# Kernel tuning notes

Measured on AMD Instinct MI355X. Metric: run time of the kernel, lower is better.

Reference implementation:

```python
import jax, jax.numpy as jnp
import numpy as np

B, S, D, N, L, V = 2, 512, 1024, 4096, 4, 32000
EPS = 1e-5

def ternarize(w):
    # BitNet b1.58-style: scale = mean |w|, quantize to {-1,0,1}, rescale.
    s = jnp.mean(jnp.abs(w)) + 1e-8
    return s * jnp.round(jnp.clip(w / s, -1.0, 1.0))

def tern_ste(w):
    # straight-through estimator (faithful to ternary training)
    return w + jax.lax.stop_gradient(ternarize(w) - w)

def layer_norm(x, g, b):
    mu = jnp.mean(x, axis=-1, keepdims=True)
    var = jnp.var(x, axis=-1, keepdims=True)
    return (x - mu) * jax.lax.rsqrt(var + EPS) * g + b

def setup_inputs() -> dict:
    key = jax.random.key(0)
    ks = jax.random.split(key, 20)
    sc = lambda d: 1.0 / np.sqrt(d)
    inp = {
        'input_ids': jax.random.randint(ks[0], (B, S), 0, V, dtype=jnp.int32),
        'emb':       jax.random.normal(ks[1], (V, D), jnp.float32) * 0.02,
        'pos_emb':   jax.random.normal(ks[2], (S, D), jnp.float32) * 0.02,
        'gru_wih':   jax.random.normal(ks[3], (3 * D, D), jnp.float32) * sc(D),
        'gru_whh':   jax.random.normal(ks[4], (3 * D, D), jnp.float32) * sc(D),
        'gru_bih':   jnp.zeros((3 * D,), jnp.float32),
        'gru_bhh':   jnp.zeros((3 * D,), jnp.float32),
        'syn_w':     jax.random.normal(ks[5], (L, N, D), jnp.float32) * sc(D),
        'syn_b':     jnp.zeros((L, N), jnp.float32),
        'out_w':     jax.random.normal(ks[6], (L, D, N), jnp.float32) * sc(N),
        'out_b':     jnp.zeros((L, D), jnp.float32),
        'ln_g':      jnp.ones((L, D), jnp.float32),
        'ln_b':      jnp.zeros((L, D), jnp.float32),
        'on_g':      jnp.ones((D,), jnp.float32),
        'on_b':      jnp.zeros((D,), jnp.float32),
        'head_w':    jax.random.normal(ks[7], (V, D), jnp.float32) * sc(D),
        'head_b':    jnp.zeros((V,), jnp.float32),
    }
    return inp

def gru(x, wih, whh, bih, bhh):
    # x: [B,S,D] -> [B,S,D], torch nn.GRU semantics, h0 = 0
    # Precompute input projections for all timesteps: [B,S,3D]
    gi_all = jnp.einsum('bsd,ed->bse', x, wih) + bih
    def step(h, gi):
        gh = h @ whh.T + bhh
        ir, iz, inn = jnp.split(gi, 3, axis=-1)
        hr, hz, hn = jnp.split(gh, 3, axis=-1)
        r = jax.nn.sigmoid(ir + hr)
        z = jax.nn.sigmoid(iz + hz)
        n = jnp.tanh(inn + r * hn)
        h_new = (1.0 - z) * n + z * h
        return h_new, h_new
    h0 = jnp.zeros((x.shape[0], whh.shape[1]), x.dtype)
    _, hs = jax.lax.scan(step, h0, jnp.swapaxes(gi_all, 0, 1))
    return jnp.swapaxes(hs, 0, 1)

def reference(input_ids, emb, pos_emb, gru_wih, gru_whh, gru_bih, gru_bhh,
              syn_w, syn_b, out_w, out_b, ln_g, ln_b, on_g, on_b,
              head_w, head_b):
    # Ternary embedding lookup
    x = tern_ste(emb)[input_ids]                       # [B,S,D]
    x = x + pos_emb[None, :x.shape[1], :]
    x = gru(x, gru_wih, gru_whh, gru_bih, gru_bhh)
    for l in range(L):
        residual = x
        hidden = jax.nn.relu(jnp.einsum('bsd,nd->bsn', x, tern_ste(syn_w[l])) + syn_b[l])
        out = jnp.einsum('bsn,dn->bsd', hidden, tern_ste(out_w[l])) + out_b[l]
        x = layer_norm(residual + out, ln_g[l], ln_b[l])
    x = layer_norm(x, on_g, on_b)
    logits = jnp.einsum('bsd,vd->bsv', x, tern_ste(head_w)) + head_b  # [B,S,V]
    return logits
```

## Files before the change

### kernel.cpp

```cpp
#include <hip/hip_runtime.h>
#include <hip/hip_bf16.h>
#include <cstdint>
#include <cstddef>

#define Dm 1024
#define Sm 512
#define Bm 2
#define Nm 4096
#define Lm 4
#define Vm 32000

typedef __attribute__((ext_vector_type(8))) short short8;
typedef __attribute__((ext_vector_type(4))) float floatx4;

__device__ __forceinline__ unsigned short f2b(float f){
  union { float f; unsigned u; } v; v.f = f;
  unsigned r = (v.u + 0x7fffu + ((v.u >> 16) & 1u)) >> 16;
  return (unsigned short)r;
}

__device__ __forceinline__ float tern_thresh(double s64){
  float T = (float)(s64 * 0.5);
  if ((double)T > s64 * 0.5) T = __uint_as_float(__float_as_uint(T) - 1u);
  return T;
}

struct AbsumArgs { const float* src[10]; long n4[10]; };

__global__ __launch_bounds__(256) void absum_all_kernel(
    AbsumArgs a, double* __restrict__ parts)
{
  int slot = blockIdx.y;
  const float* x = a.src[slot];
  long n4 = a.n4[slot];
  long i = (long)blockIdx.x * blockDim.x + threadIdx.x;
  long stride = (long)gridDim.x * blockDim.x;
  double s = 0.0;
  for (; i < n4; i += stride){
    float4 v = ((const float4*)x)[i];
    s += (double)fabsf(v.x) + (double)fabsf(v.y)
       + (double)fabsf(v.z) + (double)fabsf(v.w);
  }
  #pragma unroll
  for (int off = 32; off; off >>= 1) s += __shfl_down(s, off, 64);
  __shared__ double wsum[4];
  int lane = threadIdx.x & 63, wv = threadIdx.x >> 6;
  if (lane == 0) wsum[wv] = s;
  __syncthreads();
  if (threadIdx.x == 0)
    parts[(size_t)slot * 512 + blockIdx.x] = wsum[0]+wsum[1]+wsum[2]+wsum[3];
}

__global__ __launch_bounds__(256) void absum_final_kernel(
    const double* __restrict__ part, double* __restrict__ scales)
{
  const double* p = part + (size_t)blockIdx.x * 512;
  int tid = threadIdx.x;
  double s = p[tid] + p[tid + 256];
  #pragma unroll
  for (int off = 32; off; off >>= 1) s += __shfl_down(s, off, 64);
  __shared__ double wsum[4];
  int lane = tid & 63, wv = tid >> 6;
  if (lane == 0) wsum[wv] = s;
  __syncthreads();
  if (tid == 0) scales[blockIdx.x] = wsum[0]+wsum[1]+wsum[2]+wsum[3];
}

struct PackArgs {
  const float* src[10]; unsigned short* dst[10];
  long n4[10]; int sidx[10]; double cnt[10];
};

__global__ __launch_bounds__(256) void pack_all_kernel(
    PackArgs a, const double* __restrict__ scales)
{
  int slot = blockIdx.y;
  const float* src = a.src[slot];
  unsigned short* dst = a.dst[slot];
  long n4 = a.n4[slot];
  bool tern = (a.sidx[slot] >= 0);
  float T = 0.f;
  if (tern){
    double s64 = scales[a.sidx[slot]] / a.cnt[slot] + 1e-8;
    T = tern_thresh(s64);
  }
  long i = (long)blockIdx.x * blockDim.x + threadIdx.x;
  long stride = (long)gridDim.x * blockDim.x;
  for (; i < n4; i += stride){
    float4 v = ((const float4*)src)[i];
    ushort4 u;
    if (tern){
      u.x = (v.x > T) ? 0x3F80 : ((v.x < -T) ? 0xBF80 : 0);
      u.y = (v.y > T) ? 0x3F80 : ((v.y < -T) ? 0xBF80 : 0);
      u.z = (v.z > T) ? 0x3F80 : ((v.z < -T) ? 0xBF80 : 0);
      u.w = (v.w > T) ? 0x3F80 : ((v.w < -T) ? 0xBF80 : 0);
    } else {
      u.x = f2b(v.x); u.y = f2b(v.y); u.z = f2b(v.z); u.w = f2b(v.w);
    }
    ((ushort4*)dst)[i] = u;
  }
}

__global__ __launch_bounds__(256) void embed_kernel(
    const int* __restrict__ ids, const float* __restrict__ emb,
    const float* __restrict__ pos, const double* __restrict__ ssum,
    unsigned short* __restrict__ xb)
{
  int row = blockIdx.x;
  int sp  = row & (Sm - 1);
  int id  = ids[row];
  double s64 = ssum[0] / ((double)Vm * (double)Dm) + 1e-8;
  float s = (float)s64;
  float T = tern_thresh(s64);
  int d = threadIdx.x * 4;
  float4 wv = *(const float4*)(emb + (size_t)id * Dm + d);
  float4 pv = *(const float4*)(pos + (size_t)sp * Dm + d);
  float q0 = (wv.x > T) ? 1.f : ((wv.x < -T) ? -1.f : 0.f);
  float q1 = (wv.y > T) ? 1.f : ((wv.y < -T) ? -1.f : 0.f);
  float q2 = (wv.z > T) ? 1.f : ((wv.z < -T) ? -1.f : 0.f);
  float q3 = (wv.w > T) ? 1.f : ((wv.w < -T) ? -1.f : 0.f);
  float y0 = s * q0 + pv.x;
  float y1 = s * q1 + pv.y;
  float y2 = s * q2 + pv.z;
  float y3 = s * q3 + pv.w;
  ushort4 u = make_ushort4(f2b(y0), f2b(y1), f2b(y2), f2b(y3));
  *(ushort4*)(xb + (size_t)row * Dm + d) = u;
}

template<int WM>
__global__ __launch_bounds__(256) void gemm_t(
    const unsigned short* __restrict__ A, const void* __restrict__ Wp,
    const float* __restrict__ bias, const double* __restrict__ ssum, double cnt,
    int relu, float* __restrict__ outf, unsigned short* __restrict__ outb,
    int M, int N, int K)
{
  __shared__ unsigned short As[128][40];
  __shared__ unsigned short Bs[128][40];
  int tid = threadIdx.x;
  int wave = tid >> 6, lane = tid & 63;
  int wm = wave >> 1, wn = wave & 1;
  int bm = blockIdx.y, bn = blockIdx.x;

  float s = 1.f, T = 0.f;
  if (ssum){
    double s64 = ssum[0] / cnt + 1e-8;
    s = (float)s64;
    T = tern_thresh(s64);
  }

  int arow = tid >> 1, achunk = tid & 1;
  const unsigned short* Ag = A + (size_t)(bm * 128 + arow) * K + achunk * 16;
  const float* Wg32 = (const float*)Wp + (size_t)(bn * 128 + arow) * K + achunk * 16;
  const unsigned short* Wg16 = (const unsigned short*)Wp + (size_t)(bn * 128 + arow) * K + achunk * 16;

  floatx4 acc[4][4];
  #pragma unroll
  for (int i = 0; i < 4; i++)
    #pragma unroll
    for (int j = 0; j < 4; j++)
      acc[i][j] = (floatx4){0.f, 0.f, 0.f, 0.f};

  for (int k0 = 0; k0 < K; k0 += 32){
    __syncthreads();
    uint4 a0 = *(const uint4*)(Ag + k0);
    uint4 a1 = *(const uint4*)(Ag + k0 + 8);
    *(uint4*)&As[arow][achunk * 16]     = a0;
    *(uint4*)&As[arow][achunk * 16 + 8] = a1;
    if (WM == 2){
      uint4 b0 = *(const uint4*)(Wg16 + k0);
      uint4 b1 = *(const uint4*)(Wg16 + k0 + 8);
      *(uint4*)&Bs[arow][achunk * 16]     = b0;
      *(uint4*)&Bs[arow][achunk * 16 + 8] = b1;
    } else {
      unsigned short tmp[16];
      #pragma unroll
      for (int q = 0; q < 4; q++){
        float4 wv = *(const float4*)(Wg32 + k0 + q * 4);
        if (WM == 1){
          tmp[q*4+0] = (wv.x > T) ? 0x3F80 : ((wv.x < -T) ? 0xBF80 : 0);
          tmp[q*4+1] = (wv.y > T) ? 0x3F80 : ((wv.y < -T) ? 0xBF80 : 0);
          tmp[q*4+2] = (wv.z > T) ? 0x3F80 : ((wv.z < -T) ? 0xBF80 : 0);
          tmp[q*4+3] = (wv.w > T) ? 0x3F80 : ((wv.w < -T) ? 0xBF80 : 0);
        } else {
          tmp[q*4+0] = f2b(wv.x); tmp[q*4+1] = f2b(wv.y);
          tmp[q*4+2] = f2b(wv.z); tmp[q*4+3] = f2b(wv.w);
        }
      }
      *(uint4*)&Bs[arow][achunk * 16]     = *(uint4*)&tmp[0];
      *(uint4*)&Bs[arow][achunk * 16 + 8] = *(uint4*)&tmp[8];
    }
    __syncthreads();

    int kq = lane >> 4, mr = lane & 15;
    short8 af[4], bf[4];
    #pragma unroll
    for (int i = 0; i < 4; i++) af[i] = *(const short8*)&As[wm*64 + i*16 + mr][kq*8];
    #pragma unroll
    for (int j = 0; j < 4; j++) bf[j] = *(const short8*)&Bs[wn*64 + j*16 + mr][kq*8];
    #pragma unroll
    for (int i = 0; i < 4; i++)
      #pragma unroll
      for (int j = 0; j < 4; j++)
        acc[i][j] = __builtin_amdgcn_mfma_f32_16x16x32_bf16(af[i], bf[j], acc[i][j], 0, 0, 0);
  }

  int cr = lane >> 4, cc = lane & 15;
  #pragma unroll
  for (int j = 0; j < 4; j++){
    int col = bn * 128 + wn * 64 + j * 16 + cc;
    float bv = bias ? bias[col] : 0.f;
    #pragma unroll
    for (int i = 0; i < 4; i++){
      #pragma unroll
      for (int r = 0; r < 4; r++){
        int row = bm * 128 + wm * 64 + i * 16 + cr * 4 + r;
        float v = acc[i][j][r] * s + bv;
        if (relu) v = fmaxf(v, 0.f);
        size_t idx = (size_t)row * N + col;
        if (outf) outf[idx] = v;
        if (outb) outb[idx] = f2b(v);
      }
    }
  }
}

template<int WM>
__global__ __launch_bounds__(256) void gemm_ks_t(
    const unsigned short* __restrict__ A, const void* __restrict__ Wp,
    const float* __restrict__ bias, const double* __restrict__ ssum, double cnt,
    float* __restrict__ p0, float* __restrict__ pext,
    int M, int N, int K, int Klen)
{
  __shared__ unsigned short As[128][40];
  __shared__ unsigned short Bs[128][40];
  int tid = threadIdx.x;
  int wave = tid >> 6, lane = tid & 63;
  int wm = wave >> 1, wn = wave & 1;
  int bm = blockIdx.y, bn = blockIdx.x, z = blockIdx.z;

  float s = 1.f, T = 0.f;
  if (ssum){
    double s64 = ssum[0] / cnt + 1e-8;
    s = (float)s64;
    T = tern_thresh(s64);
  }

  int arow = tid >> 1, achunk = tid & 1;
  int kbase = z * Klen;
  const unsigned short* Ag = A + (size_t)(bm * 128 + arow) * K + kbase + achunk * 16;
  const float* Wg32 = (const float*)Wp + (size_t)(bn * 128 + arow) * K + kbase + achunk * 16;
  const unsigned short* Wg16 = (const unsigned short*)Wp + (size_t)(bn * 128 + arow) * K + kbase + achunk * 16;

  floatx4 acc[4][4];
  #pragma unroll
  for (int i = 0; i < 4; i++)
    #pragma unroll
    for (int j = 0; j < 4; j++)
      acc[i][j] = (floatx4){0.f, 0.f, 0.f, 0.f};

  for (int k0 = 0; k0 < Klen; k0 += 32){
    __syncthreads();
    uint4 a0 = *(const uint4*)(Ag + k0);
    uint4 a1 = *(const uint4*)(Ag + k0 + 8);
    *(uint4*)&As[arow][achunk * 16]     = a0;
    *(uint4*)&As[arow][achunk * 16 + 8] = a1;
    if (WM == 2){
      uint4 b0 = *(const uint4*)(Wg16 + k0);
      uint4 b1 = *(const uint4*)(Wg16 + k0 + 8);
      *(uint4*)&Bs[arow][achunk * 16]     = b0;
      *(uint4*)&Bs[arow][achunk * 16 + 8] = b1;
    } else {
      unsigned short tmp[16];
      #pragma unroll
      for (int q = 0; q < 4; q++){
        float4 wv = *(const float4*)(Wg32 + k0 + q * 4);
        tmp[q*4+0] = (wv.x > T) ? 0x3F80 : ((wv.x < -T) ? 0xBF80 : 0);
        tmp[q*4+1] = (wv.y > T) ? 0x3F80 : ((wv.y < -T) ? 0xBF80 : 0);
        tmp[q*4+2] = (wv.z > T) ? 0x3F80 : ((wv.z < -T) ? 0xBF80 : 0);
        tmp[q*4+3] = (wv.w > T) ? 0x3F80 : ((wv.w < -T) ? 0xBF80 : 0);
      }
      *(uint4*)&Bs[arow][achunk * 16]     = *(uint4*)&tmp[0];
      *(uint4*)&Bs[arow][achunk * 16 + 8] = *(uint4*)&tmp[8];
    }
    __syncthreads();

    int kq = lane >> 4, mr = lane & 15;
    short8 af[4], bf[4];
    #pragma unroll
    for (int i = 0; i < 4; i++) af[i] = *(const short8*)&As[wm*64 + i*16 + mr][kq*8];
    #pragma unroll
    for (int j = 0; j < 4; j++) bf[j] = *(const short8*)&Bs[wn*64 + j*16 + mr][kq*8];
    #pragma unroll
    for (int i = 0; i < 4; i++)
      #pragma unroll
      for (int j = 0; j < 4; j++)
        acc[i][j] = __builtin_amdgcn_mfma_f32_16x16x32_bf16(af[i], bf[j], acc[i][j], 0, 0, 0);
  }

  float* outp = (z == 0) ? p0 : pext + (size_t)(z - 1) * M * N;
  int cr = lane >> 4, cc = lane & 15;
  #pragma unroll
  for (int j = 0; j < 4; j++){
    int col = bn * 128 + wn * 64 + j * 16 + cc;
    float bv = (z == 0 && bias) ? bias[col] : 0.f;
    #pragma unroll
    for (int i = 0; i < 4; i++){
      #pragma unroll
      for (int r = 0; r < 4; r++){
        int row = bm * 128 + wm * 64 + i * 16 + cr * 4 + r;
        outp[(size_t)row * N + col] = acc[i][j][r] * s + bv;
      }
    }
  }
}

template<int WM>
__global__ __launch_bounds__(512) void gemm256_t(
    const unsigned short* __restrict__ A, const void* __restrict__ Wp,
    const float* __restrict__ bias, const double* __restrict__ ssum, double cnt,
    int relu, float* __restrict__ outf, unsigned short* __restrict__ outb,
    int M, int N, int K)
{
  __shared__ unsigned short As[256][40];
  __shared__ unsigned short Bs[128][40];
  int tid = threadIdx.x;
  int wave = tid >> 6, lane = tid & 63;
  int wm = wave >> 1, wn = wave & 1;
  int bm = blockIdx.y, bn = blockIdx.x;

  float s = 1.f, T = 0.f;
  if (ssum){
    double s64 = ssum[0] / cnt + 1e-8;
    s = (float)s64;
    T = tern_thresh(s64);
  }

  int arow = tid >> 1, achunk = tid & 1;
  int wrow = tid >> 2, wchunk = tid & 3;
  const unsigned short* Ag = A + (size_t)(bm * 256 + arow) * K + achunk * 16;
  const float* Wg32 = (const float*)Wp + (size_t)(bn * 128 + wrow) * K + wchunk * 8;
  const unsigned short* Wg16 = (const unsigned short*)Wp + (size_t)(bn * 128 + wrow) * K + wchunk * 8;

  floatx4 acc[4][4];
  #pragma unroll
  for (int i = 0; i < 4; i++)
    #pragma unroll
    for (int j = 0; j < 4; j++)
      acc[i][j] = (floatx4){0.f, 0.f, 0.f, 0.f};

  for (int k0 = 0; k0 < K; k0 += 32){
    __syncthreads();
    uint4 a0 = *(const uint4*)(Ag + k0);
    uint4 a1 = *(const uint4*)(Ag + k0 + 8);
    *(uint4*)&As[arow][achunk * 16]     = a0;
    *(uint4*)&As[arow][achunk * 16 + 8] = a1;
    if (WM == 2){
      uint4 b0 = *(const uint4*)(Wg16 + k0);
      *(uint4*)&Bs[wrow][wchunk * 8] = b0;
    } else {
      unsigned short tmp[8];
      float4 w0 = *(const float4*)(Wg32 + k0);
      float4 w1 = *(const float4*)(Wg32 + k0 + 4);
      if (WM == 1){
        tmp[0] = (w0.x > T) ? 0x3F80 : ((w0.x < -T) ? 0xBF80 : 0);
        tmp[1] = (w0.y > T) ? 0x3F80 : ((w0.y < -T) ? 0xBF80 : 0);
        tmp[2] = (w0.z > T) ? 0x3F80 : ((w0.z < -T) ? 0xBF80 : 0);
        tmp[3] = (w0.w > T) ? 0x3F80 : ((w0.w < -T) ? 0xBF80 : 0);
        tmp[4] = (w1.x > T) ? 0x3F80 : ((w1.x < -T) ? 0xBF80 : 0);
        tmp[5] = (w1.y > T) ? 0x3F80 : ((w1.y < -T) ? 0xBF80 : 0);
        tmp[6] = (w1.z > T) ? 0x3F80 : ((w1.z < -T) ? 0xBF80 : 0);
        tmp[7] = (w1.w > T) ? 0x3F80 : ((w1.w < -T) ? 0xBF80 : 0);
      } else {
        tmp[0] = f2b(w0.x); tmp[1] = f2b(w0.y); tmp[2] = f2b(w0.z); tmp[3] = f2b(w0.w);
        tmp[4] = f2b(w1.x); tmp[5] = f2b(w1.y); tmp[6] = f2b(w1.z); tmp[7] = f2b(w1.w);
      }
      *(uint2*)&Bs[wrow][wchunk * 8]     = *(uint2*)&tmp[0];
      *(uint2*)&Bs[wrow][wchunk * 8 + 4] = *(uint2*)&tmp[4];
    }
    __syncthreads();

    int kq = lane >> 4, mr = lane & 15;
    short8 af[4], bf[4];
    #pragma unroll
    for (int i = 0; i < 4; i++) af[i] = *(const short8*)&As[wm*64 + i*16 + mr][kq*8];
    #pragma unroll
    for (int j = 0; j < 4; j++) bf[j] = *(const short8*)&Bs[wn*64 + j*16 + mr][kq*8];
    #pragma unroll
    for (int i = 0; i < 4; i++)
      #pragma unroll
      for (int j = 0; j < 4; j++)
        acc[i][j] = __builtin_amdgcn_mfma_f32_16x16x32_bf16(af[i], bf[j], acc[i][j], 0, 0, 0);
  }

  int cr = lane >> 4, cc = lane & 15;
  #pragma unroll
  for (int j = 0; j < 4; j++){
    int col = bn * 128 + wn * 64 + j * 16 + cc;
    float bv = bias ? bias[col] : 0.f;
    #pragma unroll
    for (int i = 0; i < 4; i++){
      #pragma unroll
      for (int r = 0; r < 4; r++){
        int row = bm * 256 + wm * 64 + i * 16 + cr * 4 + r;
        float v = acc[i][j][r] * s + bv;
        if (relu) v = fmaxf(v, 0.f);
        size_t idx = (size_t)row * N + col;
        if (outf) outf[idx] = v;
        if (outb) outb[idx] = f2b(v);
      }
    }
  }
}

__global__ __launch_bounds__(512) void gru_kernel(
    const float* __restrict__ gi, const float* __restrict__ whh, const float* __restrict__ bhh,
    unsigned long long* __restrict__ hbuf,
    float* __restrict__ hs, unsigned short* __restrict__ hsb)
{
  __shared__ __align__(16) float lds_h[2][Dm];
  __shared__ float lds_gh[24];
  int w = blockIdx.x, tid = threadIdx.x;
  int bb = w & 1, slice = w >> 1;
  int d0 = slice * 8;
  int o = tid >> 4, c = tid & 15;
  bool active = (o < 24);
  int g = o >> 3, dl = o & 7;
  int wrow = g * Dm + d0 + dl;
  float4 wr0 = {0,0,0,0}, wr1 = wr0, wr2 = wr0, wr3 = wr0,
         wr4 = wr0, wr5 = wr0, wr6 = wr0, wr7 = wr0,
         wr8 = wr0, wr9 = wr0, wr10 = wr0, wr11 = wr0,
         wr12 = wr0, wr13 = wr0, wr14 = wr0, wr15 = wr0;
  if (active){
    const float* wsrc = whh + (size_t)wrow * Dm + c * 4;
    wr0  = *(const float4*)(wsrc +  0*64);  wr1  = *(const float4*)(wsrc +  1*64);
    wr2  = *(const float4*)(wsrc +  2*64);  wr3  = *(const float4*)(wsrc +  3*64);
    wr4  = *(const float4*)(wsrc +  4*64);  wr5  = *(const float4*)(wsrc +  5*64);
    wr6  = *(const float4*)(wsrc +  6*64);  wr7  = *(const float4*)(wsrc +  7*64);
    wr8  = *(const float4*)(wsrc +  8*64);  wr9  = *(const float4*)(wsrc +  9*64);
    wr10 = *(const float4*)(wsrc + 10*64);  wr11 = *(const float4*)(wsrc + 11*64);
    wr12 = *(const float4*)(wsrc + 12*64);  wr13 = *(const float4*)(wsrc + 13*64);
    wr14 = *(const float4*)(wsrc + 14*64);  wr15 = *(const float4*)(wsrc + 15*64);
  }
  float bhval = (active && c == 0) ? bhh[wrow] : 0.f;

  int gidx = tid * 2;
  bool self = ((tid >> 2) == slice);
  int dd = tid;
  int dth = d0 + (tid & 7);
  float pir = 0.f, piz = 0.f, pin = 0.f;
  if (tid < 8){
    const float* girow = gi + (size_t)bb * Sm * (3 * Dm);
    pir = girow[dth]; piz = girow[Dm + dth]; pin = girow[2*Dm + dth];
  }

  for (int t = 0; t < Sm; t++){
    float* lh = lds_h[t & 1];
    if (!self || t == 0){
      const unsigned long long* hsrc = hbuf + (size_t)(t & 1) * 2048 + bb * 1024 + gidx;
      unsigned long long e0, e1;
      int spins = 0;
      for (;;){
        e0 = __hip_atomic_load(hsrc + 0, __ATOMIC_RELAXED, __HIP_MEMORY_SCOPE_AGENT);
        e1 = __hip_atomic_load(hsrc + 1, __ATOMIC_RELAXED, __HIP_MEMORY_SCOPE_AGENT);
        if (((unsigned)(e0 >> 32) == (unsigned)t) &&
            ((unsigned)(e1 >> 32) == (unsigned)t)) break;
        __builtin_amdgcn_s_sleep(2);
        if (++spins > (1 << 16)) break;
      }
      lh[gidx + 0] = __uint_as_float((unsigned)e0);
      lh[gidx + 1] = __uint_as_float((unsigned)e1);
    }
    __syncthreads();
    float acc = 0.f;
    if (active){
      const float* hb = lh + c * 4;
      float4 hv;
      #define GDOT(J, W) hv = *(const float4*)(hb + (J)*64); \
          acc += W.x*hv.x + W.y*hv.y + W.z*hv.z + W.w*hv.w;
      GDOT(0,wr0)  GDOT(1,wr1)  GDOT(2,wr2)  GDOT(3,wr3)
      GDOT(4,wr4)  GDOT(5,wr5)  GDOT(6,wr6)  GDOT(7,wr7)
      GDOT(8,wr8)  GDOT(9,wr9)  GDOT(10,wr10) GDOT(11,wr11)
      GDOT(12,wr12) GDOT(13,wr13) GDOT(14,wr14) GDOT(15,wr15)
      #undef GDOT
    }
    #pragma unroll
    for (int off = 8; off; off >>= 1) acc += __shfl_xor(acc, off, 16);
    if (active && c == 0) lds_gh[o] = acc + bhval;
    __syncthreads();
    if (tid < 8){
      float gr = lds_gh[dd];
      float gz = lds_gh[8 + dd];
      float gn = lds_gh[16 + dd];
      float hv = lh[dth];
      float rr = 1.f / (1.f + expf(-(pir + gr)));
      float zz = 1.f / (1.f + expf(-(piz + gz)));
      float nn = tanhf(pin + rr * gn);
      float hnew = (1.f - zz) * nn + zz * hv;
      unsigned long long pack =
          ((unsigned long long)(unsigned)(t + 1) << 32) | (unsigned long long)__float_as_uint(hnew);
      __hip_atomic_store(hbuf + (size_t)((t + 1) & 1) * 2048 + bb * 1024 + dth, pack,
                         __ATOMIC_RELAXED, __HIP_MEMORY_SCOPE_AGENT);
      lds_h[(t + 1) & 1][dth] = hnew;
      if (t + 1 < Sm){
        const float* girow = gi + ((size_t)bb * Sm + (t+1)) * (3 * Dm);
        pir = girow[dth]; piz = girow[Dm + dth]; pin = girow[2*Dm + dth];
      }
      size_t oi = ((size_t)bb * Sm + t) * Dm + dth;
      hs[oi]  = hnew;
      hsb[oi] = f2b(hnew);
    }
  }
}

__global__ __launch_bounds__(256) void ln_kernel(
    float* __restrict__ resid, const float* __restrict__ p0,
    const float* __restrict__ pext,
    const float* __restrict__ g, const float* __restrict__ b,
    float* __restrict__ outf, unsigned short* __restrict__ outb)
{
  int row = blockIdx.x;
  int d = threadIdx.x * 4;
  size_t base = (size_t)row * Dm + d;
  float4 v = *(float4*)(resid + base);
  if (p0){
    float4 a = *(const float4*)(p0 + base);
    v.x += a.x; v.y += a.y; v.z += a.z; v.w += a.w;
  }
  if (pext){
    const size_t stride = (size_t)1024 * Dm;
    #pragma unroll
    for (int e = 0; e < 3; e++){
      float4 a = *(const float4*)(pext + e * stride + base);
      v.x += a.x; v.y += a.y; v.z += a.z; v.w += a.w;
    }
  }
  float sum = v.x + v.y + v.z + v.w;
  float sq  = v.x*v.x + v.y*v.y + v.z*v.z + v.w*v.w;
  #pragma unroll
  for (int off = 32; off; off >>= 1){
    sum += __shfl_down(sum, off, 64);
    sq  += __shfl_down(sq,  off, 64);
  }
  __shared__ float red[4][2];
  __shared__ float bc[2];
  int lane = threadIdx.x & 63, wv = threadIdx.x >> 6;
  if (lane == 0){ red[wv][0] = sum; red[wv][1] = sq; }
  __syncthreads();
  if (threadIdx.x == 0){
    float st = red[0][0] + red[1][0] + red[2][0] + red[3][0];
    float qt = red[0][1] + red[1][1] + red[2][1] + red[3][1];
    float mu = st * (1.f / Dm);
    float var = qt * (1.f / Dm) - mu * mu;
    bc[0] = mu; bc[1] = rsqrtf(var + 1e-5f);
  }
  __syncthreads();
  float mu = bc[0], rs = bc[1];
  float4 gv = *(const float4*)(g + d);
  float4 bv = *(const float4*)(b + d);
  float4 y;
  y.x = (v.x - mu) * rs * gv.x + bv.x;
  y.y = (v.y - mu) * rs * gv.y + bv.y;
  y.z = (v.z - mu) * rs * gv.z + bv.z;
  y.w = (v.w - mu) * rs * gv.w + bv.w;
  if (outf) *(float4*)(outf + base) = y;
  if (outb){
    ushort4 u = make_ushort4(f2b(y.x), f2b(y.y), f2b(y.z), f2b(y.w));
    *(ushort4*)(outb + base) = u;
  }
}

extern "C" void kernel_launch(void* const* d_in, const int* in_sizes, int n_in,
                              void* d_out, int out_size, void* d_ws, size_t ws_size,
                              hipStream_t stream)
{
  const int*   ids    = (const int*)  d_in[0];
  const float* emb    = (const float*)d_in[1];
  const float* pos    = (const float*)d_in[2];
  const float* wih    = (const float*)d_in[3];
  const float* whh    = (const float*)d_in[4];
  const float* bih    = (const float*)d_in[5];
  const float* bhh    = (const float*)d_in[6];
  const float* syn_w  = (const float*)d_in[7];
  const float* syn_b  = (const float*)d_in[8];
  const float* out_w  = (const float*)d_in[9];
  const float* out_b  = (const float*)d_in[10];
  const float* ln_g   = (const float*)d_in[11];
  const float* ln_b   = (const float*)d_in[12];
  const float* on_g   = (const float*)d_in[13];
  const float* on_b   = (const float*)d_in[14];
  const float* head_w = (const float*)d_in[15];
  const float* head_b = (const float*)d_in[16];
  float* logits = (float*)d_out;

  char* ws = (char*)d_ws;
  double*             scales = (double*)ws;
  unsigned long long* hbuf   = (unsigned long long*)(ws + 4096);
  double*             parts  = (double*)(ws + 36864);
  unsigned short*     xb     = (unsigned short*)(ws + 131072);
  float*              hs     = (float*)(ws + ((size_t)4  << 20));
  unsigned short*     hidden = (unsigned short*)(ws + ((size_t)12 << 20));
  float*              outbuf = (float*)(ws + ((size_t)20 << 20));
  float*              gi     = (float*)(ws + ((size_t)24 << 20));
  unsigned short*     wih_b  = (unsigned short*)(ws + ((size_t)36 << 20));
  unsigned short*     syn_bk = (unsigned short*)(ws + ((size_t)42 << 20));
  unsigned short*     out_bk = (unsigned short*)(ws + ((size_t)74 << 20));
  unsigned short*     head_bk= (unsigned short*)(ws + ((size_t)106 << 20));
  const size_t NEED = ((size_t)106 << 20) + (size_t)Vm * Dm * 2;
  const bool packed = (ws_size >= NEED);

  hipMemsetAsync(d_ws, 0, 36864, stream);

  const double cnt_nd = (double)Nm * (double)Dm;
  const double cnt_vd = (double)Vm * (double)Dm;

  {
    AbsumArgs aa;
    aa.src[0] = emb;    aa.n4[0] = (long)Vm * Dm / 4;
    for (int l = 0; l < Lm; l++){
      aa.src[1 + l] = syn_w + (size_t)l * Nm * Dm; aa.n4[1 + l] = (long)Nm * Dm / 4;
      aa.src[5 + l] = out_w + (size_t)l * Dm * Nm; aa.n4[5 + l] = (long)Nm * Dm / 4;
    }
    aa.src[9] = head_w; aa.n4[9] = (long)Vm * Dm / 4;
    absum_all_kernel<<<dim3(512, 10), 256, 0, stream>>>(aa, parts);
    absum_final_kernel<<<10, 256, 0, stream>>>(parts, scales);
  }

  if (packed){
    PackArgs pa;
    pa.src[0] = wih;  pa.dst[0] = wih_b;  pa.n4[0] = (long)(3*Dm)*Dm/4; pa.sidx[0] = -1; pa.cnt[0] = 1.0;
    for (int l = 0; l < Lm; l++){
      pa.src[1+l] = syn_w + (size_t)l*Nm*Dm; pa.dst[1+l] = syn_bk + (size_t)l*Nm*Dm;
      pa.n4[1+l] = (long)Nm*Dm/4; pa.sidx[1+l] = 1 + l; pa.cnt[1+l] = cnt_nd;
      pa.src[5+l] = out_w + (size_t)l*Dm*Nm; pa.dst[5+l] = out_bk + (size_t)l*Dm*Nm;
      pa.n4[5+l] = (long)Nm*Dm/4; pa.sidx[5+l] = 5 + l; pa.cnt[5+l] = cnt_nd;
    }
    pa.src[9] = head_w; pa.dst[9] = head_bk; pa.n4[9] = (long)Vm*Dm/4; pa.sidx[9] = 9; pa.cnt[9] = cnt_vd;
    pack_all_kernel<<<dim3(512, 10), 256, 0, stream>>>(pa, scales);
  }

  embed_kernel<<<1024, 256, 0, stream>>>(ids, emb, pos, scales, xb);

  if (packed)
    gemm_t<2><<<dim3(3072/128, 1024/128), 256, 0, stream>>>(
        xb, wih_b, bih, nullptr, 0.0, 0, gi, nullptr, 1024, 3072, 1024);
  else
    gemm_t<0><<<dim3(3072/128, 1024/128), 256, 0, stream>>>(
        xb, wih, bih, nullptr, 0.0, 0, gi, nullptr, 1024, 3072, 1024);

  gru_kernel<<<256, 512, 0, stream>>>(gi, whh, bhh, hbuf, hs, xb);

  for (int l = 0; l < Lm; l++){
    if (packed)
      gemm_t<2><<<dim3(4096/128, 1024/128), 256, 0, stream>>>(
          xb, syn_bk + (size_t)l * Nm * Dm, syn_b + (size_t)l * Nm,
          scales + 1 + l, cnt_nd, 1, nullptr, hidden, 1024, 4096, 1024);
    else
      gemm_t<1><<<dim3(4096/128, 1024/128), 256, 0, stream>>>(
          xb, syn_w + (size_t)l * Nm * Dm, syn_b + (size_t)l * Nm,
          scales + 1 + l, cnt_nd, 1, nullptr, hidden, 1024, 4096, 1024);
    if (packed)
      gemm_ks_t<2><<<dim3(1024/128, 1024/128, 4), 256, 0, stream>>>(
          hidden, out_bk + (size_t)l * Dm * Nm, out_b + (size_t)l * Dm,
          scales + 5 + l, cnt_nd, outbuf, gi, 1024, 1024, 4096, 1024);
    else
      gemm_ks_t<1><<<dim3(1024/128, 1024/128, 4), 256, 0, stream>>>(
          hidden, out_w + (size_t)l * Dm * Nm, out_b + (size_t)l * Dm,
          scales + 5 + l, cnt_nd, outbuf, gi, 1024, 1024, 4096, 1024);
    ln_kernel<<<1024, 256, 0, stream>>>(hs, outbuf, gi,
        ln_g + (size_t)l * Dm, ln_b + (size_t)l * Dm, hs, xb);
  }
  ln_kernel<<<1024, 256, 0, stream>>>(hs, nullptr, nullptr, on_g, on_b, nullptr, xb);

  if (packed)
    gemm256_t<2><<<dim3(32000/128, 1024/256), 512, 0, stream>>>(
        xb, head_bk, head_b, scales + 9, cnt_vd, 0, logits, nullptr, 1024, 32000, 1024);
  else
    gemm256_t<1><<<dim3(32000/128, 1024/256), 512, 0, stream>>>(
        xb, head_w, head_b, scales + 9, cnt_vd, 0, logits, nullptr, 1024, 32000, 1024);
}
```

Baseline: 2.112 ms.

## Overlap weight absum and ternary packing with GRU recurrence via extra worker blocks

Moves the abs-sum, scale reduction and ternary bf16 packing of the syn/out/head weights into extra blocks appended to the GRU kernel launch. These blocks use global atomic counters as grid barriers between phases, so weight preprocessing runs alongside the latency-bound sequential GRU instead of before it. Only the embedding scale and wih packing stay ahead of the GRU. This relies on all 400 blocks being co-resident to avoid deadlock (a spin cap is added), and the worker blocks compete with the GRU blocks for bandwidth and CUs.

```diff
diff --git a/kernel.cpp b/kernel.cpp
--- a/kernel.cpp
+++ b/kernel.cpp
@@ -9,6 +9,7 @@
 #define Nm 4096
 #define Lm 4
 #define Vm 32000
+#define NWORK 144
 
 typedef __attribute__((ext_vector_type(8))) short short8;
 typedef __attribute__((ext_vector_type(4))) float floatx4;
@@ -412,14 +413,104 @@
   }
 }
 
-__global__ __launch_bounds__(512) void gru_kernel(
+struct WPrep {
+  const float* src[9];
+  unsigned short* dst[9];
+  long n4[9];
+  double cnt[9];
+};
+
+__global__ __launch_bounds__(512, 4) void gru_fused_kernel(
     const float* __restrict__ gi, const float* __restrict__ whh, const float* __restrict__ bhh,
     unsigned long long* __restrict__ hbuf,
-    float* __restrict__ hs, unsigned short* __restrict__ hsb)
+    float* __restrict__ hs, unsigned short* __restrict__ hsb,
+    WPrep wp, double* __restrict__ parts, double* __restrict__ scales,
+    int* __restrict__ wcnt, int nwork)
 {
   __shared__ __align__(16) float lds_h[2][Dm];
   __shared__ float lds_gh[24];
-  int w = blockIdx.x, tid = threadIdx.x;
+  int tid = threadIdx.x;
+
+  if (blockIdx.x >= 256){
+    double* wsum2 = (double*)lds_h;
+    int W = blockIdx.x - 256;
+    int half = tid >> 8, t256 = tid & 255;
+    for (int vb = W * 2 + half; vb < 9 * 512; vb += nwork * 2){
+      int slot = vb >> 9, blk = vb & 511;
+      const float* x = wp.src[slot];
+      long n4 = wp.n4[slot];
+      double s = 0.0;
+      for (long i = (long)blk * 256 + t256; i < n4; i += 512 * 256){
+        float4 v = ((const float4*)x)[i];
+        s += (double)fabsf(v.x) + (double)fabsf(v.y)
+           + (double)fabsf(v.z) + (double)fabsf(v.w);
+      }
+      #pragma unroll
+      for (int off = 32; off; off >>= 1) s += __shfl_down(s, off, 64);
+      int lane = tid & 63, wv = (tid >> 6) & 3;
+      if (lane == 0) wsum2[half * 4 + wv] = s;
+      __syncthreads();
+      if (t256 == 0){
+        double tot = wsum2[half*4+0] + wsum2[half*4+1] + wsum2[half*4+2] + wsum2[half*4+3];
+        __hip_atomic_store(&parts[(size_t)(1 + slot) * 512 + blk], tot,
+                           __ATOMIC_RELAXED, __HIP_MEMORY_SCOPE_AGENT);
+      }
+      __syncthreads();
+    }
+    if (tid == 0){
+      __hip_atomic_fetch_add(wcnt, 1, __ATOMIC_ACQ_REL, __HIP_MEMORY_SCOPE_AGENT);
+      int spins = 0;
+      while (__hip_atomic_load(wcnt, __ATOMIC_ACQUIRE, __HIP_MEMORY_SCOPE_AGENT) < nwork){
+        __builtin_amdgcn_s_sleep(8);
+        if (++spins > (1 << 20)) break;
+      }
+    }
+    __syncthreads();
+    if (W < 9){
+      if (tid < 256){
+        const double* p = parts + (size_t)(1 + W) * 512;
+        double s = __hip_atomic_load(&p[tid], __ATOMIC_RELAXED, __HIP_MEMORY_SCOPE_AGENT)
+                 + __hip_atomic_load(&p[tid + 256], __ATOMIC_RELAXED, __HIP_MEMORY_SCOPE_AGENT);
+        #pragma unroll
+        for (int off = 32; off; off >>= 1) s += __shfl_down(s, off, 64);
+        int lane = tid & 63, wv = tid >> 6;
+        if (lane == 0) wsum2[wv] = s;
+      }
+      __syncthreads();
+      if (tid == 0)
+        __hip_atomic_store(&scales[1 + W], wsum2[0]+wsum2[1]+wsum2[2]+wsum2[3],
+                           __ATOMIC_RELAXED, __HIP_MEMORY_SCOPE_AGENT);
+    }
+    if (tid == 0){
+      __hip_atomic_fetch_add(wcnt + 1, 1, __ATOMIC_ACQ_REL, __HIP_MEMORY_SCOPE_AGENT);
+      int spins = 0;
+      while (__hip_atomic_load(wcnt + 1, __ATOMIC_ACQUIRE, __HIP_MEMORY_SCOPE_AGENT) < nwork){
+        __builtin_amdgcn_s_sleep(8);
+        if (++spins > (1 << 20)) break;
+      }
+    }
+    __syncthreads();
+    for (int slot = 0; slot < 9; slot++){
+      const float* src = wp.src[slot];
+      unsigned short* dst = wp.dst[slot];
+      long n4 = wp.n4[slot];
+      double sv = __hip_atomic_load(&scales[1 + slot], __ATOMIC_RELAXED, __HIP_MEMORY_SCOPE_AGENT);
+      double s64 = sv / wp.cnt[slot] + 1e-8;
+      float T = tern_thresh(s64);
+      for (long i = (long)W * 512 + tid; i < n4; i += (long)nwork * 512){
+        float4 v = ((const float4*)src)[i];
+        ushort4 u;
+        u.x = (v.x > T) ? 0x3F80 : ((v.x < -T) ? 0xBF80 : 0);
+        u.y = (v.y > T) ? 0x3F80 : ((v.y < -T) ? 0xBF80 : 0);
+        u.z = (v.z > T) ? 0x3F80 : ((v.z < -T) ? 0xBF80 : 0);
+        u.w = (v.w > T) ? 0x3F80 : ((v.w < -T) ? 0xBF80 : 0);
+        ((ushort4*)dst)[i] = u;
+      }
+    }
+    return;
+  }
+
+  int w = blockIdx.x;
   int bb = w & 1, slice = w >> 1;
   int d0 = slice * 8;
   int o = tid >> 4, c = tid & 15;
@@ -594,6 +685,7 @@
 
   char* ws = (char*)d_ws;
   double*             scales = (double*)ws;
+  int*                wcnt   = (int*)(ws + 2048);
   unsigned long long* hbuf   = (unsigned long long*)(ws + 4096);
   double*             parts  = (double*)(ws + 36864);
   unsigned short*     xb     = (unsigned short*)(ws + 131072);
@@ -613,7 +705,15 @@
   const double cnt_nd = (double)Nm * (double)Dm;
   const double cnt_vd = (double)Vm * (double)Dm;
 
-  {
+  if (packed){
+    AbsumArgs aa; aa.src[0] = emb; aa.n4[0] = (long)Vm * Dm / 4;
+    absum_all_kernel<<<dim3(512, 1), 256, 0, stream>>>(aa, parts);
+    absum_final_kernel<<<1, 256, 0, stream>>>(parts, scales);
+    PackArgs pw;
+    pw.src[0] = wih; pw.dst[0] = wih_b; pw.n4[0] = (long)(3*Dm)*Dm/4;
+    pw.sidx[0] = -1; pw.cnt[0] = 1.0;
+    pack_all_kernel<<<dim3(512, 1), 256, 0, stream>>>(pw, scales);
+  } else {
     AbsumArgs aa;
     aa.src[0] = emb;    aa.n4[0] = (long)Vm * Dm / 4;
     for (int l = 0; l < Lm; l++){
@@ -623,19 +723,6 @@
     aa.src[9] = head_w; aa.n4[9] = (long)Vm * Dm / 4;
     absum_all_kernel<<<dim3(512, 10), 256, 0, stream>>>(aa, parts);
     absum_final_kernel<<<10, 256, 0, stream>>>(parts, scales);
-  }
-
-  if (packed){
-    PackArgs pa;
-    pa.src[0] = wih;  pa.dst[0] = wih_b;  pa.n4[0] = (long)(3*Dm)*Dm/4; pa.sidx[0] = -1; pa.cnt[0] = 1.0;
-    for (int l = 0; l < Lm; l++){
-      pa.src[1+l] = syn_w + (size_t)l*Nm*Dm; pa.dst[1+l] = syn_bk + (size_t)l*Nm*Dm;
-      pa.n4[1+l] = (long)Nm*Dm/4; pa.sidx[1+l] = 1 + l; pa.cnt[1+l] = cnt_nd;
-      pa.src[5+l] = out_w + (size_t)l*Dm*Nm; pa.dst[5+l] = out_bk + (size_t)l*Dm*Nm;
-      pa.n4[5+l] = (long)Nm*Dm/4; pa.sidx[5+l] = 5 + l; pa.cnt[5+l] = cnt_nd;
-    }
-    pa.src[9] = head_w; pa.dst[9] = head_bk; pa.n4[9] = (long)Vm*Dm/4; pa.sidx[9] = 9; pa.cnt[9] = cnt_vd;
-    pack_all_kernel<<<dim3(512, 10), 256, 0, stream>>>(pa, scales);
   }
 
   embed_kernel<<<1024, 256, 0, stream>>>(ids, emb, pos, scales, xb);
@@ -647,7 +734,19 @@
     gemm_t<0><<<dim3(3072/128, 1024/128), 256, 0, stream>>>(
         xb, wih, bih, nullptr, 0.0, 0, gi, nullptr, 1024, 3072, 1024);
 
-  gru_kernel<<<256, 512, 0, stream>>>(gi, whh, bhh, hbuf, hs, xb);
+  {
+    WPrep wp;
+    for (int l = 0; l < Lm; l++){
+      wp.src[l]     = syn_w + (size_t)l * Nm * Dm; wp.dst[l]     = syn_bk + (size_t)l * Nm * Dm;
+      wp.n4[l]      = (long)Nm * Dm / 4;           wp.cnt[l]     = cnt_nd;
+      wp.src[4 + l] = out_w + (size_t)l * Dm * Nm; wp.dst[4 + l] = out_bk + (size_t)l * Dm * Nm;
+      wp.n4[4 + l]  = (long)Nm * Dm / 4;           wp.cnt[4 + l] = cnt_nd;
+    }
+    wp.src[8] = head_w; wp.dst[8] = head_bk; wp.n4[8] = (long)Vm * Dm / 4; wp.cnt[8] = cnt_vd;
+    int grid = packed ? (256 + NWORK) : 256;
+    gru_fused_kernel<<<grid, 512, 0, stream>>>(gi, whh, bhh, hbuf, hs, xb,
+                                               wp, parts, scales, wcnt, NWORK);
+  }
 
   for (int l = 0; l < Lm; l++){
     if (packed)
```

Result: slower. 2.162 ms (+2.3%).

## Overlap weight abs-sum and ternary packing with the latency-bound GRU recurrence

Applied to the files above, without the earlier changes.

Moves the abs-mean reduction and bf16 ternary packing of the syn, out and head weights into the persistent GRU kernel. Each block handles one slice of that work per timestep, hiding it behind the latency-bound serial recurrence. Cross-block reductions of partial sums go through global atomics, staged at fixed timesteps. Extra lockstep polling keeps the blocks aligned so those staged reads are valid. The risks are extra memory traffic and register pressure inside the serial loop, and a dependence on fixed timestep spacing for correctness of the cross-block reductions.

```diff
diff --git a/kernel.cpp b/kernel.cpp
--- a/kernel.cpp
+++ b/kernel.cpp
@@ -412,13 +412,18 @@
   }
 }
 
-__global__ __launch_bounds__(512) void gru_kernel(
+struct PrepPtrs { const float* src[9]; unsigned short* dst[9]; };
+
+template<bool PREP>
+__global__ __launch_bounds__(512) void gru_prep_kernel(
     const float* __restrict__ gi, const float* __restrict__ whh, const float* __restrict__ bhh,
     unsigned long long* __restrict__ hbuf,
-    float* __restrict__ hs, unsigned short* __restrict__ hsb)
+    float* __restrict__ hs, unsigned short* __restrict__ hsb,
+    PrepPtrs pp, double* __restrict__ parts, double* __restrict__ scales)
 {
   __shared__ __align__(16) float lds_h[2][Dm];
   __shared__ float lds_gh[24];
+  __shared__ double lds_aux[16];
   int w = blockIdx.x, tid = threadIdx.x;
   int bb = w & 1, slice = w >> 1;
   int d0 = slice * 8;
@@ -453,17 +458,88 @@
     pir = girow[dth]; piz = girow[Dm + dth]; pin = girow[2*Dm + dth];
   }
 
+  int myslot = 0, iters = 0, nthr = 0;
+  const float4* psrc = nullptr;
+  ushort4* pdst = nullptr;
+  double acc = 0.0, fin = 0.0;
+  float4 pend = {0.f, 0.f, 0.f, 0.f};
+  float Tq = 0.f;
+  int pbase = 0, npar = 0;
+  double mycnt = 1.0;
+  if (PREP){
+    int rank;
+    if (w < 128){ myslot = w >> 4; rank = ((w & 15) << 9) | tid; nthr = 8192;  iters = 128; }
+    else        { myslot = 8;      rank = ((w - 128) << 9) | tid; nthr = 65536; iters = 125; }
+    psrc = (const float4*)pp.src[myslot] + rank;
+    pdst = (ushort4*)pp.dst[myslot] + rank;
+    pbase = (w < 8) ? w * 16 : 128;
+    npar  = (w < 8) ? 16 : 128;
+    mycnt = (myslot == 8) ? (double)Vm * (double)Dm : (double)Nm * (double)Dm;
+    pend = psrc[0];
+  }
+
   for (int t = 0; t < Sm; t++){
+    if (PREP){
+      if (t < iters){
+        acc += (double)fabsf(pend.x) + (double)fabsf(pend.y)
+             + (double)fabsf(pend.z) + (double)fabsf(pend.w);
+        if (t + 1 < iters) pend = psrc[(size_t)(t + 1) * nthr];
+      } else if (t == 132){
+        double r = acc;
+        #pragma unroll
+        for (int off = 32; off; off >>= 1) r += __shfl_down(r, off, 64);
+        if ((tid & 63) == 0) lds_aux[tid >> 6] = r;
+        __syncthreads();
+        if (tid == 0){
+          double tot = 0.0;
+          #pragma unroll
+          for (int i = 0; i < 8; i++) tot += lds_aux[i];
+          __hip_atomic_store(&parts[w], tot, __ATOMIC_RELAXED, __HIP_MEMORY_SCOPE_AGENT);
+        }
+      } else if (t >= 140 && t < 268){
+        if (w <= 8 && tid == 0 && (t - 140) < npar)
+          fin += __hip_atomic_load(&parts[pbase + (t - 140)],
+                                   __ATOMIC_RELAXED, __HIP_MEMORY_SCOPE_AGENT);
+      } else if (t == 272){
+        if (w <= 8 && tid == 0)
+          __hip_atomic_store(&scales[1 + w], fin, __ATOMIC_RELAXED, __HIP_MEMORY_SCOPE_AGENT);
+      } else if (t == 280){
+        if (tid == 0)
+          lds_aux[9] = __hip_atomic_load(&scales[1 + myslot],
+                                         __ATOMIC_RELAXED, __HIP_MEMORY_SCOPE_AGENT);
+      } else if (t == 284){
+        double s64 = lds_aux[9] / mycnt + 1e-8;
+        Tq = tern_thresh(s64);
+        pend = psrc[0];
+      } else if (t >= 288 && t < 288 + iters){
+        int k = t - 288;
+        ushort4 u;
+        u.x = (pend.x > Tq) ? 0x3F80 : ((pend.x < -Tq) ? 0xBF80 : 0);
+        u.y = (pend.y > Tq) ? 0x3F80 : ((pend.y < -Tq) ? 0xBF80 : 0);
+        u.z = (pend.z > Tq) ? 0x3F80 : ((pend.z < -Tq) ? 0xBF80 : 0);
+        u.w = (pend.w > Tq) ? 0x3F80 : ((pend.w < -Tq) ? 0xBF80 : 0);
+        pdst[(size_t)k * nthr] = u;
+        if (k + 1 < iters) pend = psrc[(size_t)(k + 1) * nthr];
+      }
+    }
+
     float* lh = lds_h[t & 1];
     if (!self || t == 0){
       const unsigned long long* hsrc = hbuf + (size_t)(t & 1) * 2048 + bb * 1024 + gidx;
+      const unsigned long long* xsrc = hbuf + (size_t)(t & 1) * 2048 + (1 - bb) * 1024;
       unsigned long long e0, e1;
       int spins = 0;
       for (;;){
         e0 = __hip_atomic_load(hsrc + 0, __ATOMIC_RELAXED, __HIP_MEMORY_SCOPE_AGENT);
         e1 = __hip_atomic_load(hsrc + 1, __ATOMIC_RELAXED, __HIP_MEMORY_SCOPE_AGENT);
-        if (((unsigned)(e0 >> 32) == (unsigned)t) &&
-            ((unsigned)(e1 >> 32) == (unsigned)t)) break;
+        bool ok = ((unsigned)(e0 >> 32) == (unsigned)t) &&
+                  ((unsigned)(e1 >> 32) == (unsigned)t);
+        if (PREP && tid == 256){
+          unsigned long long ex =
+              __hip_atomic_load(xsrc, __ATOMIC_RELAXED, __HIP_MEMORY_SCOPE_AGENT);
+          ok = ok && ((unsigned)(ex >> 32) == (unsigned)t);
+        }
+        if (ok) break;
         __builtin_amdgcn_s_sleep(2);
         if (++spins > (1 << 16)) break;
       }
@@ -471,12 +547,12 @@
       lh[gidx + 1] = __uint_as_float((unsigned)e1);
     }
     __syncthreads();
-    float acc = 0.f;
+    float dacc = 0.f;
     if (active){
       const float* hb = lh + c * 4;
       float4 hv;
       #define GDOT(J, W) hv = *(const float4*)(hb + (J)*64); \
-          acc += W.x*hv.x + W.y*hv.y + W.z*hv.z + W.w*hv.w;
+          dacc += W.x*hv.x + W.y*hv.y + W.z*hv.z + W.w*hv.w;
       GDOT(0,wr0)  GDOT(1,wr1)  GDOT(2,wr2)  GDOT(3,wr3)
       GDOT(4,wr4)  GDOT(5,wr5)  GDOT(6,wr6)  GDOT(7,wr7)
       GDOT(8,wr8)  GDOT(9,wr9)  GDOT(10,wr10) GDOT(11,wr11)
@@ -484,8 +560,8 @@
       #undef GDOT
     }
     #pragma unroll
-    for (int off = 8; off; off >>= 1) acc += __shfl_xor(acc, off, 16);
-    if (active && c == 0) lds_gh[o] = acc + bhval;
+    for (int off = 8; off; off >>= 1) dacc += __shfl_xor(dacc, off, 16);
+    if (active && c == 0) lds_gh[o] = dacc + bhval;
     __syncthreads();
     if (tid < 8){
       float gr = lds_gh[dd];
@@ -613,7 +689,15 @@
   const double cnt_nd = (double)Nm * (double)Dm;
   const double cnt_vd = (double)Vm * (double)Dm;
 
-  {
+  if (packed){
+    AbsumArgs aa; aa.src[0] = emb; aa.n4[0] = (long)Vm * Dm / 4;
+    absum_all_kernel<<<dim3(512, 1), 256, 0, stream>>>(aa, parts);
+    absum_final_kernel<<<1, 256, 0, stream>>>(parts, scales);
+    PackArgs pw;
+    pw.src[0] = wih; pw.dst[0] = wih_b; pw.n4[0] = (long)(3*Dm)*Dm/4;
+    pw.sidx[0] = -1; pw.cnt[0] = 1.0;
+    pack_all_kernel<<<dim3(512, 1), 256, 0, stream>>>(pw, scales);
+  } else {
     AbsumArgs aa;
     aa.src[0] = emb;    aa.n4[0] = (long)Vm * Dm / 4;
     for (int l = 0; l < Lm; l++){
@@ -623,19 +707,6 @@
     aa.src[9] = head_w; aa.n4[9] = (long)Vm * Dm / 4;
     absum_all_kernel<<<dim3(512, 10), 256, 0, stream>>>(aa, parts);
     absum_final_kernel<<<10, 256, 0, stream>>>(parts, scales);
-  }
-
-  if (packed){
-    PackArgs pa;
-    pa.src[0] = wih;  pa.dst[0] = wih_b;  pa.n4[0] = (long)(3*Dm)*Dm/4; pa.sidx[0] = -1; pa.cnt[0] = 1.0;
-    for (int l = 0; l < Lm; l++){
-      pa.src[1+l] = syn_w + (size_t)l*Nm*Dm; pa.dst[1+l] = syn_bk + (size_t)l*Nm*Dm;
-      pa.n4[1+l] = (long)Nm*Dm/4; pa.sidx[1+l] = 1 + l; pa.cnt[1+l] = cnt_nd;
-      pa.src[5+l] = out_w + (size_t)l*Dm*Nm; pa.dst[5+l] = out_bk + (size_t)l*Dm*Nm;
-      pa.n4[5+l] = (long)Nm*Dm/4; pa.sidx[5+l] = 5 + l; pa.cnt[5+l] = cnt_nd;
-    }
-    pa.src[9] = head_w; pa.dst[9] = head_bk; pa.n4[9] = (long)Vm*Dm/4; pa.sidx[9] = 9; pa.cnt[9] = cnt_vd;
-    pack_all_kernel<<<dim3(512, 10), 256, 0, stream>>>(pa, scales);
   }
 
   embed_kernel<<<1024, 256, 0, stream>>>(ids, emb, pos, scales, xb);
@@ -647,7 +718,20 @@
     gemm_t<0><<<dim3(3072/128, 1024/128), 256, 0, stream>>>(
         xb, wih, bih, nullptr, 0.0, 0, gi, nullptr, 1024, 3072, 1024);
 
-  gru_kernel<<<256, 512, 0, stream>>>(gi, whh, bhh, hbuf, hs, xb);
+  {
+    PrepPtrs pp;
+    for (int l = 0; l < Lm; l++){
+      pp.src[l]     = syn_w + (size_t)l * Nm * Dm; pp.dst[l]     = syn_bk + (size_t)l * Nm * Dm;
+      pp.src[4 + l] = out_w + (size_t)l * Dm * Nm; pp.dst[4 + l] = out_bk + (size_t)l * Dm * Nm;
+    }
+    pp.src[8] = head_w; pp.dst[8] = head_bk;
+    if (packed)
+      gru_prep_kernel<true><<<256, 512, 0, stream>>>(gi, whh, bhh, hbuf, hs, xb,
+                                                     pp, parts, scales);
+    else
+      gru_prep_kernel<false><<<256, 512, 0, stream>>>(gi, whh, bhh, hbuf, hs, xb,
+                                                      pp, parts, scales);
+  }
 
   for (int l = 0; l < Lm; l++){
     if (packed)
```

Measured after the change: 1.970 ms. -6.7%, faster.
